# Optimization experiments

Measured on AMD Instinct MI355X. Metric: run time of the kernel, lower is better.

Reference implementation:

```python
import jax, jax.numpy as jnp
import numpy as np

M, K, N = 4096, 4096, 12288
GS = 128                 # quantization group size
G = K // GS              # number of groups
PACK = 8                 # int4 values per int32


def _pack_nibbles(key, shape_packed, axis_len):
    # generate random int4 values and pack 8 per int32 (bit-faithful GPTQ layout)
    nib = jax.random.randint(key, shape_packed[:1] + (PACK,) + shape_packed[1:], 0, 16, dtype=jnp.uint32)
    shifts = (jnp.arange(PACK, dtype=jnp.uint32) * 4)[None, :, None]
    return jnp.sum(nib << shifts, axis=1).astype(jnp.int32)


def setup_inputs() -> dict:
    key = jax.random.key(0)
    k1, k2, k3, k4, k5 = jax.random.split(key, 5)
    x = jax.random.normal(k1, (M, K), dtype=jnp.float32) * 0.05
    qweight = _pack_nibbles(k2, (K // PACK, N), K)          # [K/8, N] int32
    qzeros = _pack_nibbles(k3, (G, N // PACK), N)           # [G, N/8] int32
    scales = jax.random.uniform(k4, (G, N), dtype=jnp.float32, minval=0.001, maxval=0.01)
    bias = jax.random.normal(k5, (N,), dtype=jnp.float32) * 0.01
    return {"x": x, "qweight": qweight, "qzeros": qzeros, "scales": scales, "bias": bias}


def _unpack_rows(q):
    # [R, C] int32 -> [R*8, C] int4 values unpacked along rows
    shifts = (jnp.arange(PACK, dtype=jnp.uint32) * 4)[None, :, None]
    nib = (q.astype(jnp.uint32)[:, None, :] >> shifts) & jnp.uint32(0xF)
    return nib.reshape(q.shape[0] * PACK, q.shape[1])


def _unpack_cols(q):
    # [R, C] int32 -> [R, C*8] int4 values unpacked along columns
    shifts = (jnp.arange(PACK, dtype=jnp.uint32) * 4)[None, None, :]
    nib = (q.astype(jnp.uint32)[:, :, None] >> shifts) & jnp.uint32(0xF)
    return nib.reshape(q.shape[0], q.shape[1] * PACK)


def reference(x, qweight, qzeros, scales, bias):
    # dequantize: w[k,n] = (q[k,n] - (z[g,n]+1)) * s[g,n],  g = k // GS
    q = _unpack_rows(qweight).astype(jnp.float32)                    # [K, N]
    z = (_unpack_cols(qzeros).astype(jnp.float32) + 1.0)             # [G, N]
    s = scales                                                       # [G, N]
    w = (q.reshape(G, GS, N) - z[:, None, :]) * s[:, None, :]        # [G, GS, N]
    w = w.reshape(K, N)
    return x @ w + bias
```

## Files before the change

### kernel.cpp

```cpp
#include <hip/hip_runtime.h>
#include <hip/hip_bf16.h>

namespace {
constexpr int Md = 4096, Kd = 4096, Nd = 12288;
constexpr int BM = 256, BN = 256, BK = 64;
constexpr int TK = Kd / BK;
constexpr int THREADS = 512;
constexpr size_t A_BYTES = (size_t)Md * Kd * 2;
constexpr int AS_T = BM * BK;
constexpr int BS_T = BN * BK;
constexpr int LDS_BYTES = (2 * AS_T + 2 * BS_T) * 2;

typedef __attribute__((ext_vector_type(4))) float f4;
typedef __attribute__((ext_vector_type(8))) _Float16 h8;
typedef __attribute__((ext_vector_type(2))) _Float16 h2;

constexpr unsigned M4  = 0x000F000Fu;
constexpr unsigned MAG = 0x64006400u;

#define SBAR       asm volatile("s_barrier" ::: "memory")
#define WAIT_LGKM0 asm volatile("s_waitcnt lgkmcnt(0)" ::: "memory")
#define WAIT_VM0   asm volatile("s_waitcnt vmcnt(0)" ::: "memory")

__device__ __forceinline__ unsigned pkrtz(float lo, float hi) {
  return __builtin_bit_cast(unsigned, __builtin_amdgcn_cvt_pkrtz(lo, hi));
}

__global__ __launch_bounds__(256)
void cvtA_perm(const float* __restrict__ X, unsigned short* __restrict__ Xb, int n8) {
  int i = blockIdx.x * blockDim.x + threadIdx.x;
  const int stride = gridDim.x * blockDim.x;
  for (; i < n8; i += stride) {
    const f4* p = (const f4*)X + (size_t)i * 2;
    f4 a = p[0], b = p[1];
    uint4 o;
    o.x = pkrtz(a[0], b[0]); o.y = pkrtz(a[1], b[1]);
    o.z = pkrtz(a[2], b[2]); o.w = pkrtz(a[3], b[3]);
    ((uint4*)Xb)[i] = o;
  }
}

__global__ __launch_bounds__(THREADS, 2)
void qgemm8(const unsigned short* __restrict__ Xb,
            const int* __restrict__ QW, const int* __restrict__ QZ,
            const float* __restrict__ SC, const float* __restrict__ BS,
            float* __restrict__ OUT)
{
  extern __shared__ char smem[];
  unsigned short* As = (unsigned short*)smem;
  unsigned short* Bs = (unsigned short*)(smem + 2 * AS_T * 2);

  const int nwg = gridDim.x, cpx = nwg >> 3, b = blockIdx.x;
  const int swz = (b & 7) * cpx + (b >> 3);
  const int bm = swz / (Nd / BN), bn = swz % (Nd / BN);
  const int m0 = bm * BM, n0 = bn * BN;

  const int tid = threadIdx.x, lane = tid & 63, wid = tid >> 6;
  const int wr = wid >> 2, wc = wid & 3;
  const int lr = lane & 15, lk = lane >> 4;

  const int n_l = tid & 255;
  const int k8b = (tid >> 8) * 4;
  const int nab = n0 + n_l;

  f4 acc[8][4];
  #pragma unroll
  for (int i = 0; i < 8; ++i)
    #pragma unroll
    for (int j = 0; j < 4; ++j) acc[i][j] = {0.0f, 0.0f, 0.0f, 0.0f};

  h8 afr[4][2];
  h8 bfA[2][2], bfB[2][2];

  auto stageA = [&](int t, int buf, int half) {
    #pragma unroll
    for (int i = half * 2; i < half * 2 + 2; ++i) {
      const int c = i * THREADS + tid;
      const int r = c >> 3, kbl = c & 7;
      const unsigned short* src = Xb + (size_t)(m0 + r) * Kd + t * BK + ((kbl ^ (r & 7)) << 3);
      __builtin_amdgcn_global_load_lds(
          (const __attribute__((address_space(1))) unsigned*)src,
          (__attribute__((address_space(3))) unsigned*)(As + buf * AS_T + c * 8),
          16, 0, 0);
    }
  };
  auto loadQW = [&](int t, int* w) {
    const int* qp = QW + (size_t)(t * 8 + k8b) * Nd + nab;
    #pragma unroll
    for (int i = 0; i < 4; ++i) w[i] = qp[(size_t)i * Nd];
  };
  auto writeB = [&](const int* w, unsigned hs2, unsigned hz2, int buf) {
    const h2 vz = __builtin_bit_cast(h2, hz2);
    const h2 vs = __builtin_bit_cast(h2, hs2);
    #pragma unroll
    for (int i = 0; i < 4; ++i) {
      const unsigned q = (unsigned)w[i];
      const int k8 = k8b + i;
      const unsigned p0 = (q & M4) | MAG;
      const unsigned p1 = ((q >> 4) & M4) | MAG;
      const unsigned p2 = ((q >> 8) & M4) | MAG;
      const unsigned p3 = ((q >> 12) & M4) | MAG;
      const h2 f0 = (__builtin_bit_cast(h2, p0) - vz) * vs;
      const h2 f1 = (__builtin_bit_cast(h2, p1) - vz) * vs;
      const h2 f2 = (__builtin_bit_cast(h2, p2) - vz) * vs;
      const h2 f3 = (__builtin_bit_cast(h2, p3) - vz) * vs;
      uint4 o;
      o.x = __builtin_bit_cast(unsigned, f0);
      o.y = __builtin_bit_cast(unsigned, f1);
      o.z = __builtin_bit_cast(unsigned, f2);
      o.w = __builtin_bit_cast(unsigned, f3);
      *(uint4*)(Bs + buf * BS_T + n_l * BK + ((k8 ^ (n_l & 7)) << 3)) = o;
    }
  };
  auto dsA = [&](int buf, int mih) {
    const unsigned short* Ab = As + buf * AS_T;
    #pragma unroll
    for (int mi4 = 0; mi4 < 4; ++mi4) {
      const int r = wr * 128 + (mih * 4 + mi4) * 16 + lr;
      #pragma unroll
      for (int ks = 0; ks < 2; ++ks) {
        const int kb = ks * 4 + lk;
        afr[mi4][ks] = *(const h8*)&Ab[r * BK + ((kb ^ (r & 7)) << 3)];
      }
    }
  };
  auto dsB = [&](int buf, int nih, h8 (&dst)[2][2]) {
    const unsigned short* Bb = Bs + buf * BS_T;
    #pragma unroll
    for (int ni2 = 0; ni2 < 2; ++ni2) {
      const int cc = wc * 64 + (nih * 2 + ni2) * 16 + lr;
      #pragma unroll
      for (int ks = 0; ks < 2; ++ks) {
        const int kb = ks * 4 + lk;
        dst[ni2][ks] = *(const h8*)&Bb[cc * BK + ((kb ^ (cc & 7)) << 3)];
      }
    }
  };
  auto mfmaQ = [&](int mih, int nih, h8 (&bfr)[2][2]) {
    __builtin_amdgcn_s_setprio(1);
    #pragma unroll
    for (int mi4 = 0; mi4 < 4; ++mi4)
      #pragma unroll
      for (int ni2 = 0; ni2 < 2; ++ni2)
        #pragma unroll
        for (int ks = 0; ks < 2; ++ks)
          acc[mih * 4 + mi4][nih * 2 + ni2] =
            __builtin_amdgcn_mfma_f32_16x16x32_f16(afr[mi4][ks], bfr[ni2][ks],
                                                   acc[mih * 4 + mi4][nih * 2 + ni2], 0, 0, 0);
    __builtin_amdgcn_s_setprio(0);
  };
  auto makeH = [&](float s, int z32, unsigned& hs2, unsigned& hz2) {
    const int z = (z32 >> ((nab & 7) * 4)) & 15;
    hz2 = (0x6400u + (unsigned)z + 1u) * 0x10001u;
    hs2 = (unsigned)__builtin_bit_cast(unsigned short, (_Float16)s) * 0x10001u;
  };

  int bw[4];
  float sN; int zN;
  unsigned hsC, hzC;

  {
    const float s0 = SC[(size_t)0 * Nd + nab];
    const int z0 = QZ[(nab >> 3)];
    loadQW(0, bw);
    stageA(0, 0, 0); stageA(0, 0, 1);
    makeH(s0, z0, hsC, hzC);
    writeB(bw, hsC, hzC, 0);
    WAIT_LGKM0; WAIT_VM0; SBAR;
  }

  for (int u = 0; u < TK / 2; ++u) {
    const bool ns = (u < TK / 2 - 1);

    dsA(0, 0); dsB(0, 0, bfA);
    loadQW(2 * u + 1, bw);
    stageA(2 * u + 1, 1, 0);
    SBAR; mfmaQ(0, 0, bfA); SBAR;
    dsB(0, 1, bfB);
    stageA(2 * u + 1, 1, 1);
    SBAR; mfmaQ(0, 1, bfB); SBAR;
    dsA(0, 1);
    SBAR; mfmaQ(1, 0, bfA); SBAR;
    writeB(bw, hsC, hzC, 1);
    mfmaQ(1, 1, bfB);
    WAIT_LGKM0; WAIT_VM0; SBAR;

    dsA(1, 0); dsB(1, 0, bfA);
    if (ns) {
      loadQW(2 * u + 2, bw);
      sN = SC[(size_t)(u + 1) * Nd + nab];
      zN = QZ[(size_t)(u + 1) * (Nd / 8) + (nab >> 3)];
      stageA(2 * u + 2, 0, 0);
    }
    SBAR; mfmaQ(0, 0, bfA); SBAR;
    dsB(1, 1, bfB);
    if (ns) stageA(2 * u + 2, 0, 1);
    SBAR; mfmaQ(0, 1, bfB); SBAR;
    dsA(1, 1);
    SBAR; mfmaQ(1, 0, bfA); SBAR;
    if (ns) {
      unsigned nhs, nhz;
      makeH(sN, zN, nhs, nhz);
      writeB(bw, nhs, nhz, 0);
      hsC = nhs; hzC = nhz;
    }
    mfmaQ(1, 1, bfB);
    WAIT_LGKM0; WAIT_VM0; SBAR;
  }

  #pragma unroll
  for (int ni = 0; ni < 4; ++ni) {
    const int gn = n0 + wc * 64 + ni * 16 + lr;
    const float bv = BS[gn];
    #pragma unroll
    for (int mi = 0; mi < 8; ++mi) {
      const int gm = m0 + wr * 128 + mi * 16 + (lk << 2);
      #pragma unroll
      for (int j = 0; j < 4; ++j)
        OUT[(size_t)(gm + j) * Nd + gn] = acc[mi][ni][j] + bv;
    }
  }
}

__global__ __launch_bounds__(256, 2)
void qgemm_fb(const float* __restrict__ X,
              const int* __restrict__ QW, const int* __restrict__ QZ,
              const float* __restrict__ SC, const float* __restrict__ BS,
              float* __restrict__ OUT)
{
  constexpr int FBM = 256, FBN = 128;
  constexpr int FAS = FBM * BK, FBS = FBN * BK;
  extern __shared__ char smem[];
  unsigned short* As = (unsigned short*)smem;
  unsigned short* Bs = (unsigned short*)(smem + 2 * FAS * 2);

  const int nwg = gridDim.x, cpx = nwg >> 3, b = blockIdx.x;
  const int swz = (b & 7) * cpx + (b >> 3);
  const int bm = swz / (Nd / FBN), bn = swz % (Nd / FBN);
  const int m0 = bm * FBM, n0 = bn * FBN;
  const int tid = threadIdx.x, lane = tid & 63, wid = tid >> 6;
  const int wr = wid >> 1, wc = wid & 1;
  const int n_l = tid & 127;
  const int k8b = (tid >> 7) * 4;
  const int nab = n0 + n_l;

  f4 acc[8][4];
  #pragma unroll
  for (int i = 0; i < 8; ++i)
    #pragma unroll
    for (int j = 0; j < 4; ++j) acc[i][j] = {0.0f, 0.0f, 0.0f, 0.0f};

  auto stageA_f = [&](int t, int buf) {
    #pragma unroll
    for (int i = 0; i < 8; ++i) {
      const int c = i * 256 + tid;
      const int r = c >> 3, kbl = c & 7;
      const f4* src = (const f4*)(X + (size_t)(m0 + r) * Kd + t * BK + ((kbl ^ (r & 7)) << 3));
      f4 a = src[0], bb = src[1];
      uint4 o;
      o.x = pkrtz(a[0], bb[0]); o.y = pkrtz(a[1], bb[1]);
      o.z = pkrtz(a[2], bb[2]); o.w = pkrtz(a[3], bb[3]);
      *(uint4*)(As + buf * FAS + c * 8) = o;
    }
  };
  auto loadB = [&](int t, int* w, unsigned& hs2, unsigned& hz2) {
    const int* qp = QW + (size_t)(t * 8 + k8b) * Nd + nab;
    #pragma unroll
    for (int i = 0; i < 4; ++i) w[i] = qp[(size_t)i * Nd];
    const int g = t >> 1;
    const float s = SC[(size_t)g * Nd + nab];
    const int z32 = QZ[(size_t)g * (Nd / 8) + (nab >> 3)];
    const int z = (z32 >> ((nab & 7) * 4)) & 15;
    hz2 = (0x6400u + (unsigned)z + 1u) * 0x10001u;
    hs2 = (unsigned)__builtin_bit_cast(unsigned short, (_Float16)s) * 0x10001u;
  };
  auto writeB = [&](const int* w, unsigned hs2, unsigned hz2) {
    const h2 vz = __builtin_bit_cast(h2, hz2);
    const h2 vs = __builtin_bit_cast(h2, hs2);
    #pragma unroll
    for (int i = 0; i < 4; ++i) {
      const unsigned q = (unsigned)w[i];
      const int k8 = k8b + i;
      const unsigned p0 = (q & M4) | MAG;
      const unsigned p1 = ((q >> 4) & M4) | MAG;
      const unsigned p2 = ((q >> 8) & M4) | MAG;
      const unsigned p3 = ((q >> 12) & M4) | MAG;
      const h2 f0 = (__builtin_bit_cast(h2, p0) - vz) * vs;
      const h2 f1 = (__builtin_bit_cast(h2, p1) - vz) * vs;
      const h2 f2 = (__builtin_bit_cast(h2, p2) - vz) * vs;
      const h2 f3 = (__builtin_bit_cast(h2, p3) - vz) * vs;
      uint4 o;
      o.x = __builtin_bit_cast(unsigned, f0);
      o.y = __builtin_bit_cast(unsigned, f1);
      o.z = __builtin_bit_cast(unsigned, f2);
      o.w = __builtin_bit_cast(unsigned, f3);
      *(uint4*)(Bs + n_l * BK + ((k8 ^ (n_l & 7)) << 3)) = o;
    }
  };
  auto mfma_tile = [&](int cb) {
    const unsigned short* Ab = As + cb * FAS;
    #pragma unroll
    for (int ks = 0; ks < 2; ++ks) {
      h8 af[8], bf[4];
      const int kb = ks * 4 + (lane >> 4);
      #pragma unroll
      for (int mi = 0; mi < 8; ++mi) {
        const int r = wr * 128 + mi * 16 + (lane & 15);
        af[mi] = *(const h8*)&Ab[r * BK + ((kb ^ (r & 7)) << 3)];
      }
      #pragma unroll
      for (int ni = 0; ni < 4; ++ni) {
        const int cc = wc * 64 + ni * 16 + (lane & 15);
        bf[ni] = *(const h8*)&Bs[cc * BK + ((kb ^ (cc & 7)) << 3)];
      }
      #pragma unroll
      for (int mi = 0; mi < 8; ++mi)
        #pragma unroll
        for (int ni = 0; ni < 4; ++ni)
          acc[mi][ni] = __builtin_amdgcn_mfma_f32_16x16x32_f16(af[mi], bf[ni], acc[mi][ni], 0, 0, 0);
    }
  };

  int bw[4]; unsigned sHS, sHZ;
  int nbw[4]; unsigned nHS, nHZ;
  stageA_f(0, 0);
  loadB(0, bw, sHS, sHZ);
  writeB(bw, sHS, sHZ);
  __syncthreads();
  for (int t = 0; t < TK; ++t) {
    const int cb = t & 1;
    if (t + 1 < TK) loadB(t + 1, nbw, nHS, nHZ);
    mfma_tile(cb);
    __syncthreads();
    if (t + 1 < TK) {
      stageA_f(t + 1, cb ^ 1);
      writeB(nbw, nHS, nHZ);
    }
    __syncthreads();
  }
  #pragma unroll
  for (int ni = 0; ni < 4; ++ni) {
    const int gn = n0 + wc * 64 + ni * 16 + (lane & 15);
    const float bv = BS[gn];
    #pragma unroll
    for (int mi = 0; mi < 8; ++mi) {
      const int gm = m0 + wr * 128 + mi * 16 + ((lane >> 4) << 2);
      #pragma unroll
      for (int j = 0; j < 4; ++j)
        OUT[(size_t)(gm + j) * Nd + gn] = acc[mi][ni][j] + bv;
    }
  }
}
}

extern "C" void kernel_launch(void* const* d_in, const int* in_sizes, int n_in,
                              void* d_out, int out_size, void* d_ws, size_t ws_size,
                              hipStream_t stream) {
  const float* x  = (const float*)d_in[0];
  const int*   qw = (const int*)d_in[1];
  const int*   qz = (const int*)d_in[2];
  const float* sc = (const float*)d_in[3];
  const float* bs = (const float*)d_in[4];
  float* out = (float*)d_out;

  (void)hipFuncSetAttribute((const void*)qgemm8,
                            hipFuncAttributeMaxDynamicSharedMemorySize, LDS_BYTES);
  (void)hipFuncSetAttribute((const void*)qgemm_fb,
                            hipFuncAttributeMaxDynamicSharedMemorySize, (2 * 256 * BK + 128 * BK) * 2);

  if (ws_size >= A_BYTES) {
    unsigned short* xh = (unsigned short*)d_ws;
    const int n8 = Md * Kd / 8;
    cvtA_perm<<<2048, 256, 0, stream>>>(x, xh, n8);
    dim3 grid((Md / BM) * (Nd / BN));
    qgemm8<<<grid, dim3(THREADS), LDS_BYTES, stream>>>(xh, qw, qz, sc, bs, out);
  } else {
    dim3 grid((Md / 256) * (Nd / 128));
    qgemm_fb<<<grid, dim3(256), (2 * 256 * BK + 128 * BK) * 2, stream>>>(x, qw, qz, sc, bs, out);
  }
}
```

Before: 401.3 us.

## Double-register quantized weight loads and relax vmcnt waits in main loop

The packed int4 weight loads now go into two register sets (even and odd K tiles), so each load is issued one half-iteration earlier and has more compute to hide behind. Full vmcnt(0) waits become partial waits that let newer global loads stay in flight across barriers. The last iteration is peeled so the main loop carries no conditionals, and the final compute stage drops its barriers. The cost is more VGPRs for the second weight buffer, which could hurt occupancy, and the hand-counted vmcnt values must match the actual number of outstanding loads or results will be wrong.

```diff
diff --git a/kernel.cpp b/kernel.cpp
--- a/kernel.cpp
+++ b/kernel.cpp
@@ -20,7 +20,7 @@
 
 #define SBAR       asm volatile("s_barrier" ::: "memory")
 #define WAIT_LGKM0 asm volatile("s_waitcnt lgkmcnt(0)" ::: "memory")
-#define WAIT_VM0   asm volatile("s_waitcnt vmcnt(0)" ::: "memory")
+#define WAIT_VM(n) asm volatile("s_waitcnt vmcnt(" #n ")" ::: "memory")
 
 __device__ __forceinline__ unsigned pkrtz(float lo, float hi) {
   return __builtin_bit_cast(unsigned, __builtin_amdgcn_cvt_pkrtz(lo, hi));
@@ -41,7 +41,7 @@
 }
 
 __global__ __launch_bounds__(THREADS, 2)
-void qgemm8(const unsigned short* __restrict__ Xb,
+void qgemm9(const unsigned short* __restrict__ Xb,
             const int* __restrict__ QW, const int* __restrict__ QZ,
             const float* __restrict__ SC, const float* __restrict__ BS,
             float* __restrict__ OUT)
@@ -155,57 +155,84 @@
     hs2 = (unsigned)__builtin_bit_cast(unsigned short, (_Float16)s) * 0x10001u;
   };
 
-  int bw[4];
+  int wE[4], wO[4];
   float sN; int zN;
   unsigned hsC, hzC;
 
   {
-    const float s0 = SC[(size_t)0 * Nd + nab];
-    const int z0 = QZ[(nab >> 3)];
-    loadQW(0, bw);
+    loadQW(0, wE);
     stageA(0, 0, 0); stageA(0, 0, 1);
-    makeH(s0, z0, hsC, hzC);
-    writeB(bw, hsC, hzC, 0);
-    WAIT_LGKM0; WAIT_VM0; SBAR;
-  }
-
-  for (int u = 0; u < TK / 2; ++u) {
-    const bool ns = (u < TK / 2 - 1);
-
+    sN = SC[nab]; zN = QZ[nab >> 3];
+    makeH(sN, zN, hsC, hzC);
+    writeB(wE, hsC, hzC, 0);
+    loadQW(1, wO);
+    WAIT_LGKM0; WAIT_VM(4); SBAR;
+  }
+
+  for (int u = 0; u < TK / 2 - 1; ++u) {
     dsA(0, 0); dsB(0, 0, bfA);
-    loadQW(2 * u + 1, bw);
     stageA(2 * u + 1, 1, 0);
     SBAR; mfmaQ(0, 0, bfA); SBAR;
+
     dsB(0, 1, bfB);
     stageA(2 * u + 1, 1, 1);
     SBAR; mfmaQ(0, 1, bfB); SBAR;
+
+    dsA(0, 1);
+    loadQW(2 * u + 2, wE);
+    sN = SC[(size_t)(u + 1) * Nd + nab];
+    zN = QZ[(size_t)(u + 1) * (Nd / 8) + (nab >> 3)];
+    SBAR; mfmaQ(1, 0, bfA); SBAR;
+
+    writeB(wO, hsC, hzC, 1);
+    mfmaQ(1, 1, bfB);
+    WAIT_LGKM0;
+    WAIT_VM(6);
+    SBAR;
+
+    dsA(1, 0); dsB(1, 0, bfA);
+    stageA(2 * u + 2, 0, 0);
+    SBAR; mfmaQ(0, 0, bfA); SBAR;
+
+    dsB(1, 1, bfB);
+    stageA(2 * u + 2, 0, 1);
+    SBAR; mfmaQ(0, 1, bfB); SBAR;
+
+    dsA(1, 1);
+    loadQW(2 * u + 3, wO);
+    SBAR; mfmaQ(1, 0, bfA); SBAR;
+
+    makeH(sN, zN, hsC, hzC);
+    writeB(wE, hsC, hzC, 0);
+    mfmaQ(1, 1, bfB);
+    WAIT_LGKM0;
+    WAIT_VM(4);
+    SBAR;
+  }
+
+  {
+    dsA(0, 0); dsB(0, 0, bfA);
+    stageA(TK - 1, 1, 0);
+    SBAR; mfmaQ(0, 0, bfA); SBAR;
+
+    dsB(0, 1, bfB);
+    stageA(TK - 1, 1, 1);
+    SBAR; mfmaQ(0, 1, bfB); SBAR;
+
     dsA(0, 1);
     SBAR; mfmaQ(1, 0, bfA); SBAR;
-    writeB(bw, hsC, hzC, 1);
+
+    writeB(wO, hsC, hzC, 1);
     mfmaQ(1, 1, bfB);
-    WAIT_LGKM0; WAIT_VM0; SBAR;
+    WAIT_LGKM0; WAIT_VM(0); SBAR;
 
     dsA(1, 0); dsB(1, 0, bfA);
-    if (ns) {
-      loadQW(2 * u + 2, bw);
-      sN = SC[(size_t)(u + 1) * Nd + nab];
-      zN = QZ[(size_t)(u + 1) * (Nd / 8) + (nab >> 3)];
-      stageA(2 * u + 2, 0, 0);
-    }
-    SBAR; mfmaQ(0, 0, bfA); SBAR;
+    mfmaQ(0, 0, bfA);
     dsB(1, 1, bfB);
-    if (ns) stageA(2 * u + 2, 0, 1);
-    SBAR; mfmaQ(0, 1, bfB); SBAR;
+    mfmaQ(0, 1, bfB);
     dsA(1, 1);
-    SBAR; mfmaQ(1, 0, bfA); SBAR;
-    if (ns) {
-      unsigned nhs, nhz;
-      makeH(sN, zN, nhs, nhz);
-      writeB(bw, nhs, nhz, 0);
-      hsC = nhs; hzC = nhz;
-    }
+    mfmaQ(1, 0, bfA);
     mfmaQ(1, 1, bfB);
-    WAIT_LGKM0; WAIT_VM0; SBAR;
   }
 
   #pragma unroll
@@ -229,7 +256,7 @@
               float* __restrict__ OUT)
 {
   constexpr int FBM = 256, FBN = 128;
-  constexpr int FAS = FBM * BK, FBS = FBN * BK;
+  constexpr int FAS = FBM * BK;
   extern __shared__ char smem[];
   unsigned short* As = (unsigned short*)smem;
   unsigned short* Bs = (unsigned short*)(smem + 2 * FAS * 2);
@@ -363,7 +390,7 @@
   const float* bs = (const float*)d_in[4];
   float* out = (float*)d_out;
 
-  (void)hipFuncSetAttribute((const void*)qgemm8,
+  (void)hipFuncSetAttribute((const void*)qgemm9,
                             hipFuncAttributeMaxDynamicSharedMemorySize, LDS_BYTES);
   (void)hipFuncSetAttribute((const void*)qgemm_fb,
                             hipFuncAttributeMaxDynamicSharedMemorySize, (2 * 256 * BK + 128 * BK) * 2);
@@ -373,7 +400,7 @@
     const int n8 = Md * Kd / 8;
     cvtA_perm<<<2048, 256, 0, stream>>>(x, xh, n8);
     dim3 grid((Md / BM) * (Nd / BN));
-    qgemm8<<<grid, dim3(THREADS), LDS_BYTES, stream>>>(xh, qw, qz, sc, bs, out);
+    qgemm9<<<grid, dim3(THREADS), LDS_BYTES, stream>>>(xh, qw, qz, sc, bs, out);
   } else {
     dim3 grid((Md / 256) * (Nd / 128));
     qgemm_fb<<<grid, dim3(256), (2 * 256 * BK + 128 * BK) * 2, stream>>>(x, qw, qz, sc, bs, out);
```

Result: slower. 451.3 us (+12.5%).

## Dequantize int4 weights directly into MFMA registers, bypassing LDS for B

Applied to the files above, without the earlier changes.

Restructures the main GEMM so each wave loads packed int4 weights straight from global memory into registers in MFMA fragment order and dequantizes them in-register. This removes the LDS staging of B and its extra barriers. The tile shrinks to 256x128, only A stays in LDS, and occupancy is raised to 4 blocks per CU. The trade-off is that weight loads are no longer shared across the waves in a block and the hand-tuned interleaved schedule is dropped, so global weight traffic and dequant ALU work per MFMA go up.

```diff
diff --git a/kernel.cpp b/kernel.cpp
--- a/kernel.cpp
+++ b/kernel.cpp
@@ -3,13 +3,12 @@
 
 namespace {
 constexpr int Md = 4096, Kd = 4096, Nd = 12288;
-constexpr int BM = 256, BN = 256, BK = 64;
+constexpr int BM = 256, BN = 128, BK = 64;
 constexpr int TK = Kd / BK;
 constexpr int THREADS = 512;
 constexpr size_t A_BYTES = (size_t)Md * Kd * 2;
 constexpr int AS_T = BM * BK;
-constexpr int BS_T = BN * BK;
-constexpr int LDS_BYTES = (2 * AS_T + 2 * BS_T) * 2;
+constexpr int LDS_BYTES = 2 * AS_T * 2;
 
 typedef __attribute__((ext_vector_type(4))) float f4;
 typedef __attribute__((ext_vector_type(8))) _Float16 h8;
@@ -17,10 +16,6 @@
 
 constexpr unsigned M4  = 0x000F000Fu;
 constexpr unsigned MAG = 0x64006400u;
-
-#define SBAR       asm volatile("s_barrier" ::: "memory")
-#define WAIT_LGKM0 asm volatile("s_waitcnt lgkmcnt(0)" ::: "memory")
-#define WAIT_VM0   asm volatile("s_waitcnt vmcnt(0)" ::: "memory")
 
 __device__ __forceinline__ unsigned pkrtz(float lo, float hi) {
   return __builtin_bit_cast(unsigned, __builtin_amdgcn_cvt_pkrtz(lo, hi));
@@ -40,15 +35,14 @@
   }
 }
 
-__global__ __launch_bounds__(THREADS, 2)
-void qgemm8(const unsigned short* __restrict__ Xb,
-            const int* __restrict__ QW, const int* __restrict__ QZ,
-            const float* __restrict__ SC, const float* __restrict__ BS,
-            float* __restrict__ OUT)
+__global__ __launch_bounds__(THREADS, 4)
+void qgemm11(const unsigned short* __restrict__ Xb,
+             const int* __restrict__ QW, const int* __restrict__ QZ,
+             const float* __restrict__ SC, const float* __restrict__ BS,
+             float* __restrict__ OUT)
 {
   extern __shared__ char smem[];
   unsigned short* As = (unsigned short*)smem;
-  unsigned short* Bs = (unsigned short*)(smem + 2 * AS_T * 2);
 
   const int nwg = gridDim.x, cpx = nwg >> 3, b = blockIdx.x;
   const int swz = (b & 7) * cpx + (b >> 3);
@@ -59,22 +53,18 @@
   const int wr = wid >> 2, wc = wid & 3;
   const int lr = lane & 15, lk = lane >> 4;
 
-  const int n_l = tid & 255;
-  const int k8b = (tid >> 8) * 4;
-  const int nab = n0 + n_l;
-
-  f4 acc[8][4];
+  const int nqb = n0 + wc * 32 + lr;
+
+  f4 acc[8][2];
   #pragma unroll
-  for (int i = 0; i < 8; ++i)
-    #pragma unroll
-    for (int j = 0; j < 4; ++j) acc[i][j] = {0.0f, 0.0f, 0.0f, 0.0f};
-
-  h8 afr[4][2];
-  h8 bfA[2][2], bfB[2][2];
-
-  auto stageA = [&](int t, int buf, int half) {
-    #pragma unroll
-    for (int i = half * 2; i < half * 2 + 2; ++i) {
+  for (int i = 0; i < 8; ++i) {
+    acc[i][0] = {0.0f, 0.0f, 0.0f, 0.0f};
+    acc[i][1] = {0.0f, 0.0f, 0.0f, 0.0f};
+  }
+
+  auto stageA = [&](int t, int buf) {
+    #pragma unroll
+    for (int i = 0; i < 4; ++i) {
       const int c = i * THREADS + tid;
       const int r = c >> 3, kbl = c & 7;
       const unsigned short* src = Xb + (size_t)(m0 + r) * Kd + t * BK + ((kbl ^ (r & 7)) << 3);
@@ -84,133 +74,106 @@
           16, 0, 0);
     }
   };
-  auto loadQW = [&](int t, int* w) {
-    const int* qp = QW + (size_t)(t * 8 + k8b) * Nd + nab;
-    #pragma unroll
-    for (int i = 0; i < 4; ++i) w[i] = qp[(size_t)i * Nd];
-  };
-  auto writeB = [&](const int* w, unsigned hs2, unsigned hz2, int buf) {
+
+  auto loadQW = [&](int t, int* q) {
+    const int* qp = QW + (size_t)(t * 8 + lk) * Nd + nqb;
+    q[0] = qp[0];
+    q[1] = qp[16];
+    q[2] = qp[(size_t)4 * Nd];
+    q[3] = qp[(size_t)4 * Nd + 16];
+  };
+  auto loadSZ = [&](int g, float* s, int* z32) {
+    #pragma unroll
+    for (int ni = 0; ni < 2; ++ni) {
+      const int n_i = nqb + ni * 16;
+      s[ni] = SC[(size_t)g * Nd + n_i];
+      z32[ni] = QZ[(size_t)g * (Nd / 8) + (n_i >> 3)];
+    }
+  };
+  auto makeH = [&](const float* s, const int* z32, unsigned* hs, unsigned* hz) {
+    #pragma unroll
+    for (int ni = 0; ni < 2; ++ni) {
+      const int n_i = nqb + ni * 16;
+      const int z = (z32[ni] >> ((n_i & 7) * 4)) & 15;
+      hz[ni] = (0x6400u + (unsigned)z + 1u) * 0x10001u;
+      hs[ni] = (unsigned)__builtin_bit_cast(unsigned short, (_Float16)s[ni]) * 0x10001u;
+    }
+  };
+  auto deq = [&](unsigned q, unsigned hs2, unsigned hz2) -> h8 {
     const h2 vz = __builtin_bit_cast(h2, hz2);
     const h2 vs = __builtin_bit_cast(h2, hs2);
-    #pragma unroll
-    for (int i = 0; i < 4; ++i) {
-      const unsigned q = (unsigned)w[i];
-      const int k8 = k8b + i;
-      const unsigned p0 = (q & M4) | MAG;
-      const unsigned p1 = ((q >> 4) & M4) | MAG;
-      const unsigned p2 = ((q >> 8) & M4) | MAG;
-      const unsigned p3 = ((q >> 12) & M4) | MAG;
-      const h2 f0 = (__builtin_bit_cast(h2, p0) - vz) * vs;
-      const h2 f1 = (__builtin_bit_cast(h2, p1) - vz) * vs;
-      const h2 f2 = (__builtin_bit_cast(h2, p2) - vz) * vs;
-      const h2 f3 = (__builtin_bit_cast(h2, p3) - vz) * vs;
-      uint4 o;
-      o.x = __builtin_bit_cast(unsigned, f0);
-      o.y = __builtin_bit_cast(unsigned, f1);
-      o.z = __builtin_bit_cast(unsigned, f2);
-      o.w = __builtin_bit_cast(unsigned, f3);
-      *(uint4*)(Bs + buf * BS_T + n_l * BK + ((k8 ^ (n_l & 7)) << 3)) = o;
-    }
-  };
-  auto dsA = [&](int buf, int mih) {
+    const unsigned p0 = (q & M4) | MAG;
+    const unsigned p1 = ((q >> 4) & M4) | MAG;
+    const unsigned p2 = ((q >> 8) & M4) | MAG;
+    const unsigned p3 = ((q >> 12) & M4) | MAG;
+    const h2 f0 = (__builtin_bit_cast(h2, p0) - vz) * vs;
+    const h2 f1 = (__builtin_bit_cast(h2, p1) - vz) * vs;
+    const h2 f2 = (__builtin_bit_cast(h2, p2) - vz) * vs;
+    const h2 f3 = (__builtin_bit_cast(h2, p3) - vz) * vs;
+    uint4 o;
+    o.x = __builtin_bit_cast(unsigned, f0);
+    o.y = __builtin_bit_cast(unsigned, f1);
+    o.z = __builtin_bit_cast(unsigned, f2);
+    o.w = __builtin_bit_cast(unsigned, f3);
+    return __builtin_bit_cast(h8, o);
+  };
+
+  auto compute = [&](int buf, const int* q, const unsigned* hs, const unsigned* hz) {
     const unsigned short* Ab = As + buf * AS_T;
     #pragma unroll
-    for (int mi4 = 0; mi4 < 4; ++mi4) {
-      const int r = wr * 128 + (mih * 4 + mi4) * 16 + lr;
-      #pragma unroll
-      for (int ks = 0; ks < 2; ++ks) {
-        const int kb = ks * 4 + lk;
-        afr[mi4][ks] = *(const h8*)&Ab[r * BK + ((kb ^ (r & 7)) << 3)];
+    for (int ks = 0; ks < 2; ++ks) {
+      const int kb = ks * 4 + lk;
+      h8 bq0 = deq((unsigned)q[ks * 2 + 0], hs[0], hz[0]);
+      h8 bq1 = deq((unsigned)q[ks * 2 + 1], hs[1], hz[1]);
+      #pragma unroll
+      for (int mih = 0; mih < 2; ++mih) {
+        h8 af[4];
+        #pragma unroll
+        for (int mi4 = 0; mi4 < 4; ++mi4) {
+          const int r = wr * 128 + (mih * 4 + mi4) * 16 + lr;
+          af[mi4] = *(const h8*)&Ab[r * BK + ((kb ^ (r & 7)) << 3)];
+        }
+        #pragma unroll
+        for (int mi4 = 0; mi4 < 4; ++mi4) {
+          acc[mih * 4 + mi4][0] =
+            __builtin_amdgcn_mfma_f32_16x16x32_f16(af[mi4], bq0, acc[mih * 4 + mi4][0], 0, 0, 0);
+          acc[mih * 4 + mi4][1] =
+            __builtin_amdgcn_mfma_f32_16x16x32_f16(af[mi4], bq1, acc[mih * 4 + mi4][1], 0, 0, 0);
+        }
       }
     }
   };
-  auto dsB = [&](int buf, int nih, h8 (&dst)[2][2]) {
-    const unsigned short* Bb = Bs + buf * BS_T;
-    #pragma unroll
-    for (int ni2 = 0; ni2 < 2; ++ni2) {
-      const int cc = wc * 64 + (nih * 2 + ni2) * 16 + lr;
-      #pragma unroll
-      for (int ks = 0; ks < 2; ++ks) {
-        const int kb = ks * 4 + lk;
-        dst[ni2][ks] = *(const h8*)&Bb[cc * BK + ((kb ^ (cc & 7)) << 3)];
-      }
-    }
-  };
-  auto mfmaQ = [&](int mih, int nih, h8 (&bfr)[2][2]) {
-    __builtin_amdgcn_s_setprio(1);
-    #pragma unroll
-    for (int mi4 = 0; mi4 < 4; ++mi4)
-      #pragma unroll
-      for (int ni2 = 0; ni2 < 2; ++ni2)
-        #pragma unroll
-        for (int ks = 0; ks < 2; ++ks)
-          acc[mih * 4 + mi4][nih * 2 + ni2] =
-            __builtin_amdgcn_mfma_f32_16x16x32_f16(afr[mi4][ks], bfr[ni2][ks],
-                                                   acc[mih * 4 + mi4][nih * 2 + ni2], 0, 0, 0);
-    __builtin_amdgcn_s_setprio(0);
-  };
-  auto makeH = [&](float s, int z32, unsigned& hs2, unsigned& hz2) {
-    const int z = (z32 >> ((nab & 7) * 4)) & 15;
-    hz2 = (0x6400u + (unsigned)z + 1u) * 0x10001u;
-    hs2 = (unsigned)__builtin_bit_cast(unsigned short, (_Float16)s) * 0x10001u;
-  };
-
-  int bw[4];
-  float sN; int zN;
-  unsigned hsC, hzC;
-
-  {
-    const float s0 = SC[(size_t)0 * Nd + nab];
-    const int z0 = QZ[(nab >> 3)];
-    loadQW(0, bw);
-    stageA(0, 0, 0); stageA(0, 0, 1);
-    makeH(s0, z0, hsC, hzC);
-    writeB(bw, hsC, hzC, 0);
-    WAIT_LGKM0; WAIT_VM0; SBAR;
-  }
+
+  int qA[4], qB[4];
+  float sC[2]; int zC[2];
+  unsigned hs[2], hz[2];
+
+  loadSZ(0, sC, zC);
+  loadQW(0, qA);
+  stageA(0, 0);
+  makeH(sC, zC, hs, hz);
+  __syncthreads();
 
   for (int u = 0; u < TK / 2; ++u) {
     const bool ns = (u < TK / 2 - 1);
-
-    dsA(0, 0); dsB(0, 0, bfA);
-    loadQW(2 * u + 1, bw);
-    stageA(2 * u + 1, 1, 0);
-    SBAR; mfmaQ(0, 0, bfA); SBAR;
-    dsB(0, 1, bfB);
-    stageA(2 * u + 1, 1, 1);
-    SBAR; mfmaQ(0, 1, bfB); SBAR;
-    dsA(0, 1);
-    SBAR; mfmaQ(1, 0, bfA); SBAR;
-    writeB(bw, hsC, hzC, 1);
-    mfmaQ(1, 1, bfB);
-    WAIT_LGKM0; WAIT_VM0; SBAR;
-
-    dsA(1, 0); dsB(1, 0, bfA);
+    stageA(2 * u + 1, 1);
+    loadQW(2 * u + 1, qB);
+    if (ns) loadSZ(u + 1, sC, zC);
+    compute(0, qA, hs, hz);
+    __syncthreads();
+
     if (ns) {
-      loadQW(2 * u + 2, bw);
-      sN = SC[(size_t)(u + 1) * Nd + nab];
-      zN = QZ[(size_t)(u + 1) * (Nd / 8) + (nab >> 3)];
-      stageA(2 * u + 2, 0, 0);
-    }
-    SBAR; mfmaQ(0, 0, bfA); SBAR;
-    dsB(1, 1, bfB);
-    if (ns) stageA(2 * u + 2, 0, 1);
-    SBAR; mfmaQ(0, 1, bfB); SBAR;
-    dsA(1, 1);
-    SBAR; mfmaQ(1, 0, bfA); SBAR;
-    if (ns) {
-      unsigned nhs, nhz;
-      makeH(sN, zN, nhs, nhz);
-      writeB(bw, nhs, nhz, 0);
-      hsC = nhs; hzC = nhz;
-    }
-    mfmaQ(1, 1, bfB);
-    WAIT_LGKM0; WAIT_VM0; SBAR;
+      stageA(2 * u + 2, 0);
+      loadQW(2 * u + 2, qA);
+    }
+    compute(1, qB, hs, hz);
+    if (ns) makeH(sC, zC, hs, hz);
+    __syncthreads();
   }
 
   #pragma unroll
-  for (int ni = 0; ni < 4; ++ni) {
-    const int gn = n0 + wc * 64 + ni * 16 + lr;
+  for (int ni = 0; ni < 2; ++ni) {
+    const int gn = n0 + wc * 32 + ni * 16 + lr;
     const float bv = BS[gn];
     #pragma unroll
     for (int mi = 0; mi < 8; ++mi) {
@@ -229,7 +192,7 @@
               float* __restrict__ OUT)
 {
   constexpr int FBM = 256, FBN = 128;
-  constexpr int FAS = FBM * BK, FBS = FBN * BK;
+  constexpr int FAS = FBM * BK;
   extern __shared__ char smem[];
   unsigned short* As = (unsigned short*)smem;
   unsigned short* Bs = (unsigned short*)(smem + 2 * FAS * 2);
@@ -363,19 +326,18 @@
   const float* bs = (const float*)d_in[4];
   float* out = (float*)d_out;
 
-  (void)hipFuncSetAttribute((const void*)qgemm8,
+  (void)hipFuncSetAttribute((const void*)qgemm11,
                             hipFuncAttributeMaxDynamicSharedMemorySize, LDS_BYTES);
   (void)hipFuncSetAttribute((const void*)qgemm_fb,
                             hipFuncAttributeMaxDynamicSharedMemorySize, (2 * 256 * BK + 128 * BK) * 2);
 
+  dim3 grid((Md / BM) * (Nd / BN));
   if (ws_size >= A_BYTES) {
     unsigned short* xh = (unsigned short*)d_ws;
     const int n8 = Md * Kd / 8;
     cvtA_perm<<<2048, 256, 0, stream>>>(x, xh, n8);
-    dim3 grid((Md / BM) * (Nd / BN));
-    qgemm8<<<grid, dim3(THREADS), LDS_BYTES, stream>>>(xh, qw, qz, sc, bs, out);
+    qgemm11<<<grid, dim3(THREADS), LDS_BYTES, stream>>>(xh, qw, qz, sc, bs, out);
   } else {
-    dim3 grid((Md / 256) * (Nd / 128));
     qgemm_fb<<<grid, dim3(256), (2 * 256 * BK + 128 * BK) * 2, stream>>>(x, qw, qz, sc, bs, out);
   }
 }
```

Result: slower. 592.0 us (+47.5%).

## Shrink GEMM tile to 128x128 with simpler double-buffered pipeline

Applied to the files above, without the earlier changes.

Cuts the main int4-dequant GEMM tile from 256x256 with 512 threads down to 128x128 with 256 threads. The hand-interleaved ds_read/MFMA schedule with explicit s_barrier and setprio is replaced by a plain per-buffer mfma_tile loop using __syncthreads, and quantized-weight loads are prefetched one tile further ahead. Smaller tiles should let more workgroups run per CU and shorten the per-block tail, but each block now reuses A and B data less, so global and LDS traffic per FLOP goes up.

```diff
diff --git a/kernel.cpp b/kernel.cpp
--- a/kernel.cpp
+++ b/kernel.cpp
@@ -3,9 +3,9 @@
 
 namespace {
 constexpr int Md = 4096, Kd = 4096, Nd = 12288;
-constexpr int BM = 256, BN = 256, BK = 64;
+constexpr int BM = 128, BN = 128, BK = 64;
 constexpr int TK = Kd / BK;
-constexpr int THREADS = 512;
+constexpr int THREADS = 256;
 constexpr size_t A_BYTES = (size_t)Md * Kd * 2;
 constexpr int AS_T = BM * BK;
 constexpr int BS_T = BN * BK;
@@ -17,10 +17,6 @@
 
 constexpr unsigned M4  = 0x000F000Fu;
 constexpr unsigned MAG = 0x64006400u;
-
-#define SBAR       asm volatile("s_barrier" ::: "memory")
-#define WAIT_LGKM0 asm volatile("s_waitcnt lgkmcnt(0)" ::: "memory")
-#define WAIT_VM0   asm volatile("s_waitcnt vmcnt(0)" ::: "memory")
 
 __device__ __forceinline__ unsigned pkrtz(float lo, float hi) {
   return __builtin_bit_cast(unsigned, __builtin_amdgcn_cvt_pkrtz(lo, hi));
@@ -41,10 +37,10 @@
 }
 
 __global__ __launch_bounds__(THREADS, 2)
-void qgemm8(const unsigned short* __restrict__ Xb,
-            const int* __restrict__ QW, const int* __restrict__ QZ,
-            const float* __restrict__ SC, const float* __restrict__ BS,
-            float* __restrict__ OUT)
+void qgemm12(const unsigned short* __restrict__ Xb,
+             const int* __restrict__ QW, const int* __restrict__ QZ,
+             const float* __restrict__ SC, const float* __restrict__ BS,
+             float* __restrict__ OUT)
 {
   extern __shared__ char smem[];
   unsigned short* As = (unsigned short*)smem;
@@ -56,25 +52,22 @@
   const int m0 = bm * BM, n0 = bn * BN;
 
   const int tid = threadIdx.x, lane = tid & 63, wid = tid >> 6;
-  const int wr = wid >> 2, wc = wid & 3;
+  const int wr = wid >> 1, wc = wid & 1;
   const int lr = lane & 15, lk = lane >> 4;
 
-  const int n_l = tid & 255;
-  const int k8b = (tid >> 8) * 4;
+  const int n_l = tid & 127;
+  const int k8b = (tid >> 7) * 4;
   const int nab = n0 + n_l;
 
-  f4 acc[8][4];
+  f4 acc[4][4];
   #pragma unroll
-  for (int i = 0; i < 8; ++i)
+  for (int i = 0; i < 4; ++i)
     #pragma unroll
     for (int j = 0; j < 4; ++j) acc[i][j] = {0.0f, 0.0f, 0.0f, 0.0f};
 
-  h8 afr[4][2];
-  h8 bfA[2][2], bfB[2][2];
-
-  auto stageA = [&](int t, int buf, int half) {
-    #pragma unroll
-    for (int i = half * 2; i < half * 2 + 2; ++i) {
+  auto stageA = [&](int t, int buf) {
+    #pragma unroll
+    for (int i = 0; i < 4; ++i) {
       const int c = i * THREADS + tid;
       const int r = c >> 3, kbl = c & 7;
       const unsigned short* src = Xb + (size_t)(m0 + r) * Kd + t * BK + ((kbl ^ (r & 7)) << 3);
@@ -112,42 +105,29 @@
       *(uint4*)(Bs + buf * BS_T + n_l * BK + ((k8 ^ (n_l & 7)) << 3)) = o;
     }
   };
-  auto dsA = [&](int buf, int mih) {
-    const unsigned short* Ab = As + buf * AS_T;
-    #pragma unroll
-    for (int mi4 = 0; mi4 < 4; ++mi4) {
-      const int r = wr * 128 + (mih * 4 + mi4) * 16 + lr;
-      #pragma unroll
-      for (int ks = 0; ks < 2; ++ks) {
-        const int kb = ks * 4 + lk;
-        afr[mi4][ks] = *(const h8*)&Ab[r * BK + ((kb ^ (r & 7)) << 3)];
+  auto mfma_tile = [&](int cb) {
+    const unsigned short* Ab = As + cb * AS_T;
+    const unsigned short* Bb = Bs + cb * BS_T;
+    #pragma unroll
+    for (int ks = 0; ks < 2; ++ks) {
+      h8 af[4], bf[4];
+      const int kb = ks * 4 + lk;
+      #pragma unroll
+      for (int mi = 0; mi < 4; ++mi) {
+        const int r = wr * 64 + mi * 16 + lr;
+        af[mi] = *(const h8*)&Ab[r * BK + ((kb ^ (r & 7)) << 3)];
       }
-    }
-  };
-  auto dsB = [&](int buf, int nih, h8 (&dst)[2][2]) {
-    const unsigned short* Bb = Bs + buf * BS_T;
-    #pragma unroll
-    for (int ni2 = 0; ni2 < 2; ++ni2) {
-      const int cc = wc * 64 + (nih * 2 + ni2) * 16 + lr;
-      #pragma unroll
-      for (int ks = 0; ks < 2; ++ks) {
-        const int kb = ks * 4 + lk;
-        dst[ni2][ks] = *(const h8*)&Bb[cc * BK + ((kb ^ (cc & 7)) << 3)];
+      #pragma unroll
+      for (int ni = 0; ni < 4; ++ni) {
+        const int cc = wc * 64 + ni * 16 + lr;
+        bf[ni] = *(const h8*)&Bb[cc * BK + ((kb ^ (cc & 7)) << 3)];
       }
-    }
-  };
-  auto mfmaQ = [&](int mih, int nih, h8 (&bfr)[2][2]) {
-    __builtin_amdgcn_s_setprio(1);
-    #pragma unroll
-    for (int mi4 = 0; mi4 < 4; ++mi4)
-      #pragma unroll
-      for (int ni2 = 0; ni2 < 2; ++ni2)
+      #pragma unroll
+      for (int mi = 0; mi < 4; ++mi)
         #pragma unroll
-        for (int ks = 0; ks < 2; ++ks)
-          acc[mih * 4 + mi4][nih * 2 + ni2] =
-            __builtin_amdgcn_mfma_f32_16x16x32_f16(afr[mi4][ks], bfr[ni2][ks],
-                                                   acc[mih * 4 + mi4][nih * 2 + ni2], 0, 0, 0);
-    __builtin_amdgcn_s_setprio(0);
+        for (int ni = 0; ni < 4; ++ni)
+          acc[mi][ni] = __builtin_amdgcn_mfma_f32_16x16x32_f16(af[mi], bf[ni], acc[mi][ni], 0, 0, 0);
+    }
   };
   auto makeH = [&](float s, int z32, unsigned& hs2, unsigned& hz2) {
     const int z = (z32 >> ((nab & 7) * 4)) & 15;
@@ -155,57 +135,44 @@
     hs2 = (unsigned)__builtin_bit_cast(unsigned short, (_Float16)s) * 0x10001u;
   };
 
-  int bw[4];
+  int wE[4], wO[4];
   float sN; int zN;
   unsigned hsC, hzC;
 
+  loadQW(0, wE);
+  stageA(0, 0);
   {
-    const float s0 = SC[(size_t)0 * Nd + nab];
-    const int z0 = QZ[(nab >> 3)];
-    loadQW(0, bw);
-    stageA(0, 0, 0); stageA(0, 0, 1);
+    const float s0 = SC[nab];
+    const int z0 = QZ[nab >> 3];
     makeH(s0, z0, hsC, hzC);
-    writeB(bw, hsC, hzC, 0);
-    WAIT_LGKM0; WAIT_VM0; SBAR;
-  }
+  }
+  writeB(wE, hsC, hzC, 0);
+  loadQW(1, wO);
+  __syncthreads();
 
   for (int u = 0; u < TK / 2; ++u) {
     const bool ns = (u < TK / 2 - 1);
 
-    dsA(0, 0); dsB(0, 0, bfA);
-    loadQW(2 * u + 1, bw);
-    stageA(2 * u + 1, 1, 0);
-    SBAR; mfmaQ(0, 0, bfA); SBAR;
-    dsB(0, 1, bfB);
-    stageA(2 * u + 1, 1, 1);
-    SBAR; mfmaQ(0, 1, bfB); SBAR;
-    dsA(0, 1);
-    SBAR; mfmaQ(1, 0, bfA); SBAR;
-    writeB(bw, hsC, hzC, 1);
-    mfmaQ(1, 1, bfB);
-    WAIT_LGKM0; WAIT_VM0; SBAR;
-
-    dsA(1, 0); dsB(1, 0, bfA);
+    stageA(2 * u + 1, 1);
+    writeB(wO, hsC, hzC, 1);
     if (ns) {
-      loadQW(2 * u + 2, bw);
+      loadQW(2 * u + 2, wE);
       sN = SC[(size_t)(u + 1) * Nd + nab];
       zN = QZ[(size_t)(u + 1) * (Nd / 8) + (nab >> 3)];
-      stageA(2 * u + 2, 0, 0);
-    }
-    SBAR; mfmaQ(0, 0, bfA); SBAR;
-    dsB(1, 1, bfB);
-    if (ns) stageA(2 * u + 2, 0, 1);
-    SBAR; mfmaQ(0, 1, bfB); SBAR;
-    dsA(1, 1);
-    SBAR; mfmaQ(1, 0, bfA); SBAR;
+    }
+    mfma_tile(0);
+    __syncthreads();
+
     if (ns) {
+      stageA(2 * u + 2, 0);
       unsigned nhs, nhz;
       makeH(sN, zN, nhs, nhz);
-      writeB(bw, nhs, nhz, 0);
+      writeB(wE, nhs, nhz, 0);
       hsC = nhs; hzC = nhz;
-    }
-    mfmaQ(1, 1, bfB);
-    WAIT_LGKM0; WAIT_VM0; SBAR;
+      loadQW(2 * u + 3, wO);
+    }
+    mfma_tile(1);
+    __syncthreads();
   }
 
   #pragma unroll
@@ -213,8 +180,8 @@
     const int gn = n0 + wc * 64 + ni * 16 + lr;
     const float bv = BS[gn];
     #pragma unroll
-    for (int mi = 0; mi < 8; ++mi) {
-      const int gm = m0 + wr * 128 + mi * 16 + (lk << 2);
+    for (int mi = 0; mi < 4; ++mi) {
+      const int gm = m0 + wr * 64 + mi * 16 + (lk << 2);
       #pragma unroll
       for (int j = 0; j < 4; ++j)
         OUT[(size_t)(gm + j) * Nd + gn] = acc[mi][ni][j] + bv;
@@ -229,7 +196,7 @@
               float* __restrict__ OUT)
 {
   constexpr int FBM = 256, FBN = 128;
-  constexpr int FAS = FBM * BK, FBS = FBN * BK;
+  constexpr int FAS = FBM * BK;
   extern __shared__ char smem[];
   unsigned short* As = (unsigned short*)smem;
   unsigned short* Bs = (unsigned short*)(smem + 2 * FAS * 2);
@@ -363,7 +330,7 @@
   const float* bs = (const float*)d_in[4];
   float* out = (float*)d_out;
 
-  (void)hipFuncSetAttribute((const void*)qgemm8,
+  (void)hipFuncSetAttribute((const void*)qgemm12,
                             hipFuncAttributeMaxDynamicSharedMemorySize, LDS_BYTES);
   (void)hipFuncSetAttribute((const void*)qgemm_fb,
                             hipFuncAttributeMaxDynamicSharedMemorySize, (2 * 256 * BK + 128 * BK) * 2);
@@ -373,7 +340,7 @@
     const int n8 = Md * Kd / 8;
     cvtA_perm<<<2048, 256, 0, stream>>>(x, xh, n8);
     dim3 grid((Md / BM) * (Nd / BN));
-    qgemm8<<<grid, dim3(THREADS), LDS_BYTES, stream>>>(xh, qw, qz, sc, bs, out);
+    qgemm12<<<grid, dim3(THREADS), LDS_BYTES, stream>>>(xh, qw, qz, sc, bs, out);
   } else {
     dim3 grid((Md / 256) * (Nd / 128));
     qgemm_fb<<<grid, dim3(256), (2 * 256 * BK + 128 * BK) * 2, stream>>>(x, qw, qz, sc, bs, out);
```

After: 549.6 us. 37.0% more time.
